# Performance work log

Measured on AMD Instinct MI355X. Metric: run time of the kernel, lower is better.

The kernel has to match this reference:

```python
import jax, jax.numpy as jnp
import numpy as np

B, T, D = 32, 512, 384
DUR_MAX = 8                 # durations drawn in [0, DUR_MAX)
MAX_OUT = T * (DUR_MAX - 1) # static upper bound on total expanded length (3584)
ALPHA = 1.0


def setup_inputs() -> dict:
    key = jax.random.key(0)
    k1, k2 = jax.random.split(key)
    x = jax.random.normal(k1, (B, T, D), dtype=jnp.float32)
    durations = jax.random.randint(k2, (B, T), 0, DUR_MAX, dtype=jnp.int32)
    return {"input": x, "durations": durations}


def reference(input, durations):
    # patched_dur = clamp(round(alpha * dur), min=0)
    patched = jnp.round(ALPHA * durations.astype(jnp.float32)).astype(jnp.int32)
    patched = jnp.maximum(patched, 0)                       # [B, T]
    cum = jnp.cumsum(patched, axis=1)                       # [B, T] exclusive-right boundaries
    total = cum[:, -1:]                                      # [B, 1] true expanded lengths

    pos = jnp.arange(MAX_OUT, dtype=jnp.int32)               # [MAX_OUT]
    # output frame j comes from token idx = first t with cum[t] > j
    idx = jax.vmap(lambda c: jnp.searchsorted(c, pos, side='right'))(cum)  # [B, MAX_OUT]
    idx = jnp.clip(idx, 0, T - 1)
    valid = pos[None, :] < total                              # [B, MAX_OUT]

    out = jnp.take_along_axis(input, idx[:, :, None], axis=1)  # [B, MAX_OUT, D]
    return jnp.where(valid[:, :, None], out, jnp.zeros((), dtype=input.dtype))
```

## Files before the change

kernel.cpp:

```cpp
#include <hip/hip_runtime.h>

#define NB 32
#define NT 512
#define ND 384
#define DUR_MAX 8
#define MAX_OUT (NT * (DUR_MAX - 1))
#define NV (ND / 4)

__global__ __launch_bounds__(NT) void lr_scan_scatter(
    const int* __restrict__ dur, int* __restrict__ totals, int* __restrict__ idxmap)
{
    __shared__ int s[NT];
    const int b = blockIdx.x;
    const int t = threadIdx.x;

    int d = dur[b * NT + t];
    d = d > 0 ? d : 0;
    s[t] = d;
    __syncthreads();

    #pragma unroll
    for (int off = 1; off < NT; off <<= 1) {
        int v = (t >= off) ? s[t - off] : 0;
        __syncthreads();
        s[t] += v;
        __syncthreads();
    }
    const int cum = s[t];
    const int start = cum - d;

    int* base = idxmap + b * MAX_OUT;
    for (int j = 0; j < d; ++j) base[start + j] = t;

    if (t == NT - 1) totals[b] = cum;
}

__global__ __launch_bounds__(256) void lr_gather(
    const float4* __restrict__ in, const int* __restrict__ totals,
    const int* __restrict__ idxmap, float4* __restrict__ out)
{
    const unsigned g = blockIdx.x * 256u + threadIdx.x;
    const unsigned row = g / NV;
    const unsigned col = g - row * NV;
    const unsigned b = row / MAX_OUT;
    const unsigned pos = row - b * MAX_OUT;

    float4 r = make_float4(0.f, 0.f, 0.f, 0.f);
    if ((int)pos < totals[b]) {
        const int idx = idxmap[row];
        r = in[(b * NT + idx) * NV + col];
    }
    out[g] = r;
}

extern "C" void kernel_launch(void* const* d_in, const int* in_sizes, int n_in,
                              void* d_out, int out_size, void* d_ws, size_t ws_size,
                              hipStream_t stream)
{
    const float* x   = (const float*)d_in[0];
    const int*   dur = (const int*)d_in[1];
    float* out = (float*)d_out;

    int* totals = (int*)d_ws;
    int* idxmap = (int*)((char*)d_ws + 128);

    lr_scan_scatter<<<NB, NT, 0, stream>>>(dur, totals, idxmap);

    const unsigned n_vec = (unsigned)NB * MAX_OUT * NV;
    lr_gather<<<n_vec / 256, 256, 0, stream>>>(
        (const float4*)x, totals, idxmap, (float4*)out);
}
```

Measured before the change: 204.1 us.

## Gather two float4 per thread with nontemporal stores and XCD-aware block swizzle

The gather kernel now has each thread copy two adjacent 16-byte vectors instead of one, halving the thread count. Output writes use nontemporal stores so the large streaming output does not pollute cache. Block IDs are remapped in groups of eight so consecutive logical blocks land on the same XCD, which improves L2 locality for the source reads. These changes reduce index overhead and cache contention, but give up some memory-level parallelism per thread.

```diff
diff --git a/kernel.cpp b/kernel.cpp
--- a/kernel.cpp
+++ b/kernel.cpp
@@ -1,11 +1,14 @@
 #include <hip/hip_runtime.h>
+
+typedef float v4f __attribute__((ext_vector_type(4)));
 
 #define NB 32
 #define NT 512
 #define ND 384
-#define DUR_MAX 8
-#define MAX_OUT (NT * (DUR_MAX - 1))
+#define MAX_OUT 3584
 #define NV (ND / 4)
+#define TPR (NV / 2)
+#define BLK 256
 
 __global__ __launch_bounds__(NT) void lr_scan_scatter(
     const int* __restrict__ dur, int* __restrict__ totals, int* __restrict__ idxmap)
@@ -35,22 +38,32 @@
     if (t == NT - 1) totals[b] = cum;
 }
 
-__global__ __launch_bounds__(256) void lr_gather(
-    const float4* __restrict__ in, const int* __restrict__ totals,
-    const int* __restrict__ idxmap, float4* __restrict__ out)
+__global__ __launch_bounds__(BLK) void lr_gather2(
+    const v4f* __restrict__ in, const int* __restrict__ totals,
+    const int* __restrict__ idxmap, v4f* __restrict__ out)
 {
-    const unsigned g = blockIdx.x * 256u + threadIdx.x;
-    const unsigned row = g / NV;
-    const unsigned col = g - row * NV;
-    const unsigned b = row / MAX_OUT;
+    const unsigned g8 = gridDim.x >> 3;
+    const unsigned nb = (blockIdx.x & 7u) * g8 + (blockIdx.x >> 3);
+    const unsigned g  = nb * BLK + threadIdx.x;
+
+    const unsigned row = g / TPR;
+    const unsigned col = g - row * TPR;
+    const unsigned b   = row / MAX_OUT;
     const unsigned pos = row - b * MAX_OUT;
 
-    float4 r = make_float4(0.f, 0.f, 0.f, 0.f);
-    if ((int)pos < totals[b]) {
-        const int idx = idxmap[row];
-        r = in[(b * NT + idx) * NV + col];
+    const int tot = totals[b];
+    const int idx = idxmap[row];
+
+    v4f r0 = {0.f, 0.f, 0.f, 0.f};
+    v4f r1 = {0.f, 0.f, 0.f, 0.f};
+    if ((int)pos < tot) {
+        const v4f* src = in + (unsigned)(b * NT + idx) * NV + col * 2u;
+        r0 = src[0];
+        r1 = src[1];
     }
-    out[g] = r;
+    v4f* dst = out + (size_t)g * 2u;
+    __builtin_nontemporal_store(r0, dst);
+    __builtin_nontemporal_store(r1, dst + 1);
 }
 
 extern "C" void kernel_launch(void* const* d_in, const int* in_sizes, int n_in,
@@ -59,14 +72,13 @@
 {
     const float* x   = (const float*)d_in[0];
     const int*   dur = (const int*)d_in[1];
-    float* out = (float*)d_out;
 
     int* totals = (int*)d_ws;
     int* idxmap = (int*)((char*)d_ws + 128);
 
     lr_scan_scatter<<<NB, NT, 0, stream>>>(dur, totals, idxmap);
 
-    const unsigned n_vec = (unsigned)NB * MAX_OUT * NV;
-    lr_gather<<<n_vec / 256, 256, 0, stream>>>(
-        (const float4*)x, totals, idxmap, (float4*)out);
+    const unsigned n_thr = (unsigned)NB * MAX_OUT * TPR;
+    lr_gather2<<<n_thr / BLK, BLK, 0, stream>>>(
+        (const v4f*)x, totals, idxmap, (v4f*)d_out);
 }
```

After: 216.2 us. +5.9%, slower.
